# Kernel tuning notes

Hardware: AMD Instinct MI355X
Metric: run time of the kernel (lower is better)

Reference implementation:

```python
import jax, jax.numpy as jnp
import numpy as np

B, N, M = 16, 2048, 2048


def setup_inputs() -> dict:
    key = jax.random.key(0)
    k1, k2, k3 = jax.random.split(key, 3)
    pred_dsmat = jax.random.uniform(k1, (B, N, M), dtype=jnp.float32)
    # valid sizes: src_ns <= tgt_ns so a permutation GT exists for every valid row
    src_ns = jax.random.randint(k2, (B,), 1024, 1537, dtype=jnp.int32)
    tgt_ns = jax.random.randint(k3, (B,), 1537, 2049, dtype=jnp.int32)
    # gt_perm: identity permutation restricted to the valid region (one 1 per valid row)
    i = jnp.arange(N)[:, None]
    j = jnp.arange(M)[None, :]
    eye = (i == j).astype(jnp.float32)  # [N, M]
    row_mask = (jnp.arange(N)[None, :] < src_ns[:, None]).astype(jnp.float32)  # [B, N]
    gt_perm = eye[None, :, :] * row_mask[:, :, None]  # [B, N, M]
    return {"pred_dsmat": pred_dsmat, "gt_perm": gt_perm,
            "src_ns": src_ns, "tgt_ns": tgt_ns, "beta_value": 0.1}


def reference(pred_dsmat, gt_perm, src_ns, tgt_ns, beta_value):
    Bn, Nn, Mn = pred_dsmat.shape
    row_mask = jnp.arange(Nn)[None, :] < src_ns[:, None]   # [B, N] bool
    col_mask = jnp.arange(Mn)[None, :] < tgt_ns[:, None]   # [B, M] bool
    mask = row_mask[:, :, None] & col_mask[:, None, :]     # [B, N, M]

    pred = jnp.clip(pred_dsmat, 0.0, 1.0) * mask
    gt = gt_perm * mask

    gt_pred = pred * gt                      # gt-selected predicted values
    row_gt = gt_pred.sum(axis=2)             # [B, N] per-row GT value
    col_gt = gt_pred.sum(axis=1)             # [B, M] per-col GT value
    row_cnt = gt.sum(axis=2)                 # [B, N] #GT matches per row
    col_cnt = gt.sum(axis=1)                 # [B, M] #GT matches per col

    # attention masks: entries >= (gt value - beta), restricted to valid region
    att_src = ((pred >= row_gt[:, :, None] - beta_value) & mask) * row_cnt[:, :, None]
    att_tgt = ((pred >= col_gt[:, None, :] - beta_value) & mask) * col_cnt[:, None, :]

    src_neg = jnp.sum(((att_src - gt) * pred) ** 2, axis=2)  # [B, N]
    src_pos = jnp.sum(gt_pred ** 2, axis=2)                  # [B, N]
    tgt_neg = jnp.sum(((att_tgt - gt) * pred) ** 2, axis=1)  # [B, M]

    # sum of tgt_neg over the GT-matched column of each row == dot with column counts
    corr = jnp.einsum('bm,bm->b', tgt_neg, col_cnt)          # [B]

    denom = 1.0 + src_neg + corr[:, None]                    # [B, N]
    num = jnp.where(row_mask, src_pos, 1.0)
    den = jnp.where(row_mask, denom, 1.0)
    loss = -0.5 * jnp.sum(jnp.log(num / den) * row_mask)
    n_sum = src_ns.sum().astype(pred.dtype)
    return loss / n_sum
```

## Files before the change

### kernel.cpp

```cpp
#include <hip/hip_runtime.h>

#define B_ 16
#define N_ 2048
#define M_ 2048
#define RROWS 16
#define WROWS 4
#define CHUNK 1024
#define NCHUNK (M_ / CHUNK)
#define JCH (CHUNK / 256)
#define DROWS 32
#define DWROWS 8
#define KCAP 4

__device__ __forceinline__ float wave_sum(float v) {
#pragma unroll
    for (int off = 32; off >= 1; off >>= 1) v += __shfl_xor(v, off);
    return v;
}

extern "C" __global__ __launch_bounds__(256) void k_gt(
    const float* __restrict__ gt,
    const int* __restrict__ src_ns, const int* __restrict__ tgt_ns,
    int* __restrict__ nnz, int* __restrict__ ent_col,
    float* __restrict__ ent_val, int* flag)
{
    const int b = blockIdx.y;
    const int src = src_ns[b];
    const int band = blockIdx.x;
    if (band * RROWS >= src) return;
    const int tgt = tgt_ns[b];
    const int c0 = blockIdx.z * CHUNK;
    const int lim = tgt - c0;
    if (lim <= 0) return;
    const int jmaxL = lim >= CHUNK ? JCH : ((lim + 255) >> 8);
    const int wave = threadIdx.x >> 6, lane = threadIdx.x & 63;
    const int bc = b * (N_ * M_) + c0;

    const int row0 = band * RROWS + wave * WROWS;
    for (int r = 0; r < WROWS; ++r) {
        const int n = row0 + r;
        if (n >= src) break;
        const int ri = b * N_ + n;
        const float4* grow = (const float4*)(gt + bc + n * M_);
        for (int j = 0; j < jmaxL; ++j) {
            const int m4 = j * 64 + lane;
            const float4 g4 = grow[m4];
            if (g4.x != 0.f || g4.y != 0.f || g4.z != 0.f || g4.w != 0.f) {
                const int mb = c0 + m4 * 4;
#define GC(KK, MB) do { \
    const int c = mb + KK; \
    const float gv = g4.MB; \
    if (gv != 0.f && c < tgt) { \
        const int slot = atomicAdd(&nnz[ri], 1); \
        if (slot < KCAP) { ent_col[ri * KCAP + slot] = c; ent_val[ri * KCAP + slot] = gv; } \
        else *flag = 1; \
    } \
} while (0)
                GC(0, x); GC(1, y); GC(2, z); GC(3, w);
#undef GC
            }
        }
    }
}

extern "C" __global__ __launch_bounds__(256) void k_mid(
    const float* __restrict__ pred,
    const int* __restrict__ src_ns,
    const int* __restrict__ nnz, const int* __restrict__ ent_col,
    const float* __restrict__ ent_val, const int* flag,
    float* __restrict__ row_gt, float* __restrict__ row_cnt,
    float* __restrict__ col_gt, float* __restrict__ col_cnt)
{
    if (*flag) return;
    const int ri = blockIdx.x * 256 + threadIdx.x;
    const int b = ri >> 11, n = ri & (N_ - 1);
    if (n >= src_ns[b]) { row_gt[ri] = 0.f; row_cnt[ri] = 0.f; return; }
    const int nn0 = nnz[ri];
    const int nn = nn0 < KCAP ? nn0 : KCAP;
    float rg = 0.f, rc = 0.f;
    for (int s = 0; s < nn; ++s) {
        const int c = ent_col[ri * KCAP + s];
        const float gv = ent_val[ri * KCAP + s];
        float p = pred[b * (N_ * M_) + n * M_ + c];
        p = fminf(fmaxf(p, 0.f), 1.f);
        rg += gv * p; rc += gv;
        atomicAdd(&col_gt[b * M_ + c], gv * p);
        atomicAdd(&col_cnt[b * M_ + c], gv);
    }
    row_gt[ri] = rg; row_cnt[ri] = rc;
}

extern "C" __global__ __launch_bounds__(256) void k_p1d(
    const float* __restrict__ pred, const float* __restrict__ gt,
    const int* __restrict__ src_ns, const int* __restrict__ tgt_ns,
    const int* flag,
    float* __restrict__ row_gt, float* __restrict__ row_cnt,
    float* __restrict__ col_gt, float* __restrict__ col_cnt)
{
    if (*flag == 0) return;
    const int b = blockIdx.y;
    const int src = src_ns[b];
    const int band = blockIdx.x;
    if (band * DROWS >= src) return;
    const int tgt = tgt_ns[b];
    const int wave = threadIdx.x >> 6, lane = threadIdx.x & 63;
    const int base = b * (N_ * M_);

    float4 acg[8], accn[8];
#pragma unroll
    for (int j = 0; j < 8; ++j) { acg[j] = make_float4(0,0,0,0); accn[j] = make_float4(0,0,0,0); }

    const int row0 = band * DROWS + wave * DWROWS;
    for (int r = 0; r < DWROWS; ++r) {
        const int n = row0 + r;
        if (n >= src) break;
        const float4* prow = (const float4*)(pred + base + n * M_);
        const float4* grow = (const float4*)(gt + base + n * M_);
        float rg = 0.f, rc = 0.f;
#pragma unroll
        for (int j = 0; j < 8; ++j) {
            const int m4 = j * 64 + lane;
            const float4 p4 = prow[m4];
            const float4 g4 = grow[m4];
            const int mb = m4 * 4;
#define P1C(KK, MB) do { \
    const bool ok = (mb + KK) < tgt; \
    float p = fminf(fmaxf(p4.MB, 0.f), 1.f); p = ok ? p : 0.f; \
    const float g = ok ? g4.MB : 0.f; \
    const float gp = p * g; \
    rg += gp; rc += g; \
    acg[j].MB += gp; accn[j].MB += g; \
} while (0)
            P1C(0, x); P1C(1, y); P1C(2, z); P1C(3, w);
#undef P1C
        }
        rg = wave_sum(rg); rc = wave_sum(rc);
        if (lane == 0) { row_gt[b * N_ + n] = rg; row_cnt[b * N_ + n] = rc; }
    }

    __shared__ float4 s_cg[M_ / 4];
    __shared__ float4 s_cc[M_ / 4];
    for (int i = threadIdx.x; i < M_ / 4; i += 256) {
        s_cg[i] = make_float4(0,0,0,0);
        s_cc[i] = make_float4(0,0,0,0);
    }
    __syncthreads();
    for (int w = 0; w < 4; ++w) {
        if (wave == w) {
#pragma unroll
            for (int j = 0; j < 8; ++j) {
                const int i = j * 64 + lane;
                float4 v = s_cg[i];
                v.x += acg[j].x; v.y += acg[j].y; v.z += acg[j].z; v.w += acg[j].w;
                s_cg[i] = v;
                float4 u = s_cc[i];
                u.x += accn[j].x; u.y += accn[j].y; u.z += accn[j].z; u.w += accn[j].w;
                s_cc[i] = u;
            }
        }
        __syncthreads();
    }
    const float* fcg = (const float*)s_cg;
    const float* fcc = (const float*)s_cc;
    for (int i = threadIdx.x; i < M_; i += 256) {
        atomicAdd(&col_gt[b * M_ + i], fcg[i]);
        atomicAdd(&col_cnt[b * M_ + i], fcc[i]);
    }
}

extern "C" __global__ __launch_bounds__(256) void k_pred(
    const float* __restrict__ pred, const float* __restrict__ gt,
    const int* __restrict__ src_ns, const int* __restrict__ tgt_ns,
    const float* __restrict__ beta_p,
    const float* __restrict__ row_gt, const float* __restrict__ row_cnt,
    const float* __restrict__ col_gt, const float* __restrict__ col_cnt,
    const int* __restrict__ nnz, const int* __restrict__ ent_col,
    const float* __restrict__ ent_val, const int* flag,
    float* __restrict__ src_neg, float* __restrict__ src_pos,
    float* __restrict__ tgt_neg)
{
    const int b = blockIdx.y;
    const int src = src_ns[b];
    const int band = blockIdx.x;
    if (band * RROWS >= src) return;
    const int tgt = tgt_ns[b];
    const int c0 = blockIdx.z * CHUNK;
    const bool chunk0 = (c0 == 0);
    const int lim = tgt - c0;
    if (lim <= 0 && !chunk0) return;
    const int jmaxL = lim >= CHUNK ? JCH : (lim > 0 ? ((lim + 255) >> 8) : 0);
    const float beta = beta_p[0];
    const int wave = threadIdx.x >> 6, lane = threadIdx.x & 63;
    const int bfull = b * (N_ * M_);
    const int bc = bfull + c0;
    const bool dense = (*flag != 0);

    float4 cgb[JCH], cc[JCH], tn[JCH];
    const float4* cg4 = (const float4*)(col_gt + b * M_ + c0);
    const float4* cc4 = (const float4*)(col_cnt + b * M_ + c0);
#pragma unroll
    for (int j = 0; j < JCH; ++j) {
        float4 v = cg4[j * 64 + lane];
        v.x -= beta; v.y -= beta; v.z -= beta; v.w -= beta;
        cgb[j] = v;
        cc[j] = cc4[j * 64 + lane];
        tn[j] = make_float4(0,0,0,0);
    }

    const int row0 = band * RROWS + wave * WROWS;
    if (!dense) {
        for (int r = 0; r < WROWS; ++r) {
            const int n = row0 + r;
            if (n >= src) break;
            const int ri = b * N_ + n;
            const float rc = row_cnt[ri];
            const float rth = row_gt[ri] - beta;
            const float4* prow = (const float4*)(pred + bc + n * M_);
            float sneg = 0.f;
#pragma unroll
            for (int j = 0; j < JCH; ++j) {
                if (j < jmaxL) {
                    const int m4 = j * 64 + lane;
                    const float4 p4 = prow[m4];
                    const int mb = c0 + m4 * 4;
#define P2S(KK, MB) do { \
    const bool ok = (mb + KK) < tgt; \
    float p = fminf(fmaxf(p4.MB, 0.f), 1.f); p = ok ? p : 0.f; \
    const float as = (p >= rth) ? rc : 0.f; \
    const float ds = as * p; \
    sneg += ds * ds; \
    const float at = (p >= cgb[j].MB) ? cc[j].MB : 0.f; \
    const float d = at * p; \
    tn[j].MB += d * d; \
} while (0)
                    P2S(0, x); P2S(1, y); P2S(2, z); P2S(3, w);
#undef P2S
                }
            }
            sneg = wave_sum(sneg);
            if (lane == 0) {
                if (chunk0) {
                    float spos = 0.f;
                    const int nn0 = nnz[ri];
                    const int nn = nn0 < KCAP ? nn0 : KCAP;
                    for (int s = 0; s < nn; ++s) {
                        const int c = ent_col[ri * KCAP + s];
                        const float gv = ent_val[ri * KCAP + s];
                        float pv = pred[bfull + n * M_ + c];
                        pv = fminf(fmaxf(pv, 0.f), 1.f);
                        const float as = (pv >= rth) ? rc : 0.f;
                        const float d0 = as * pv;
                        const float d1 = (as - gv) * pv;
                        sneg += d1 * d1 - d0 * d0;
                        const float gp = gv * pv;
                        spos += gp * gp;
                        const float at = (pv >= col_gt[b * M_ + c] - beta) ? col_cnt[b * M_ + c] : 0.f;
                        const float t0 = at * pv;
                        const float t1 = (at - gv) * pv;
                        atomicAdd(&tgt_neg[b * M_ + c], t1 * t1 - t0 * t0);
                    }
                    atomicAdd(&src_pos[ri], spos);
                }
                atomicAdd(&src_neg[ri], sneg);
            }
        }
    } else {
        for (int r = 0; r < WROWS; ++r) {
            const int n = row0 + r;
            if (n >= src) break;
            const int ri = b * N_ + n;
            const float rc = row_cnt[ri];
            const float rth = row_gt[ri] - beta;
            const float4* prow = (const float4*)(pred + bc + n * M_);
            const float4* grow = (const float4*)(gt + bc + n * M_);
            float sneg = 0.f, spos = 0.f;
#pragma unroll
            for (int j = 0; j < JCH; ++j) {
                if (j < jmaxL) {
                    const int m4 = j * 64 + lane;
                    const float4 p4 = prow[m4];
                    const float4 g4 = grow[m4];
                    const int mb = c0 + m4 * 4;
#define P2D(KK, MB) do { \
    const bool ok = (mb + KK) < tgt; \
    float p = fminf(fmaxf(p4.MB, 0.f), 1.f); p = ok ? p : 0.f; \
    const float gv = ok ? g4.MB : 0.f; \
    const float as = (p >= rth) ? rc : 0.f; \
    const float ds = (as - gv) * p; \
    sneg += ds * ds; \
    const float gp = gv * p; spos += gp * gp; \
    const float at = (p >= cgb[j].MB) ? cc[j].MB : 0.f; \
    const float dt = (at - gv) * p; \
    tn[j].MB += dt * dt; \
} while (0)
                    P2D(0, x); P2D(1, y); P2D(2, z); P2D(3, w);
#undef P2D
                }
            }
            sneg = wave_sum(sneg); spos = wave_sum(spos);
            if (lane == 0) {
                atomicAdd(&src_neg[ri], sneg);
                atomicAdd(&src_pos[ri], spos);
            }
        }
    }

    __shared__ float4 s_tn[CHUNK / 4];
    for (int i = threadIdx.x; i < CHUNK / 4; i += 256) s_tn[i] = make_float4(0,0,0,0);
    __syncthreads();
    for (int w = 0; w < 4; ++w) {
        if (wave == w) {
#pragma unroll
            for (int j = 0; j < JCH; ++j) {
                const int i = j * 64 + lane;
                float4 v = s_tn[i];
                v.x += tn[j].x; v.y += tn[j].y; v.z += tn[j].z; v.w += tn[j].w;
                s_tn[i] = v;
            }
        }
        __syncthreads();
    }
    const float* ftn = (const float*)s_tn;
    for (int i = threadIdx.x; i < CHUNK; i += 256)
        atomicAdd(&tgt_neg[b * M_ + c0 + i], ftn[i]);
}

extern "C" __global__ __launch_bounds__(256) void k_final(
    const float* __restrict__ src_neg, const float* __restrict__ src_pos,
    const float* __restrict__ tgt_neg, const float* __restrict__ col_cnt,
    const int* __restrict__ src_ns, float* __restrict__ out)
{
    const int b = blockIdx.x;
    const int wave = threadIdx.x >> 6, lane = threadIdx.x & 63;
    __shared__ float sredc[4];
    __shared__ float sredl[4];

    float c = 0.f;
    for (int i = threadIdx.x; i < M_; i += 256)
        c += tgt_neg[b * M_ + i] * col_cnt[b * M_ + i];
    c = wave_sum(c);
    if (lane == 0) sredc[wave] = c;
    __syncthreads();
    const float corr = sredc[0] + sredc[1] + sredc[2] + sredc[3];

    const int src = src_ns[b];
    float ls = 0.f;
    for (int n = threadIdx.x; n < src; n += 256) {
        const float sp = src_pos[b * N_ + n];
        const float sn = src_neg[b * N_ + n];
        ls += logf(sp) - logf(1.f + sn + corr);
    }
    ls = wave_sum(ls);
    if (lane == 0) sredl[wave] = ls;
    __syncthreads();
    if (threadIdx.x == 0) {
        const float total = sredl[0] + sredl[1] + sredl[2] + sredl[3];
        float nsum = 0.f;
        for (int i = 0; i < B_; ++i) nsum += (float)src_ns[i];
        atomicAdd(out, -0.5f * total / nsum);
    }
}

extern "C" void kernel_launch(void* const* d_in, const int* in_sizes, int n_in,
                              void* d_out, int out_size, void* d_ws, size_t ws_size,
                              hipStream_t stream)
{
    const float* pred   = (const float*)d_in[0];
    const float* gtp    = (const float*)d_in[1];
    const int*   src_ns = (const int*)d_in[2];
    const int*   tgt_ns = (const int*)d_in[3];
    const float* beta   = (const float*)d_in[4];
    float* out = (float*)d_out;
    float* ws  = (float*)d_ws;

    float* col_gt  = ws;
    float* col_cnt = col_gt  + B_ * M_;
    float* tgt_neg = col_cnt + B_ * M_;
    float* src_neg = tgt_neg + B_ * M_;
    float* src_pos = src_neg + B_ * N_;
    int*   nnz     = (int*)(src_pos + B_ * N_);
    int*   flag    = nnz + B_ * N_;
    float* row_gt  = (float*)(flag + 1);
    float* row_cnt = row_gt + B_ * N_;
    int*   ent_col = (int*)(row_cnt + B_ * N_);
    float* ent_val = (float*)(ent_col + B_ * N_ * KCAP);

    const size_t zero_bytes = (size_t)(3 * B_ * M_ + 3 * B_ * N_ + 1) * sizeof(float);
    hipMemsetAsync(d_ws, 0, zero_bytes, stream);
    hipMemsetAsync(d_out, 0, sizeof(float), stream);

    dim3 gsplit(N_ / RROWS, B_, NCHUNK);
    k_gt<<<gsplit, 256, 0, stream>>>(gtp, src_ns, tgt_ns, nnz, ent_col, ent_val, flag);
    k_mid<<<(B_ * N_) / 256, 256, 0, stream>>>(pred, src_ns, nnz, ent_col, ent_val, flag,
                                               row_gt, row_cnt, col_gt, col_cnt);
    k_p1d<<<dim3(N_ / DROWS, B_), 256, 0, stream>>>(pred, gtp, src_ns, tgt_ns, flag,
                                                    row_gt, row_cnt, col_gt, col_cnt);
    k_pred<<<gsplit, 256, 0, stream>>>(pred, gtp, src_ns, tgt_ns, beta,
                                       row_gt, row_cnt, col_gt, col_cnt,
                                       nnz, ent_col, ent_val, flag,
                                       src_neg, src_pos, tgt_neg);
    k_final<<<B_, 256, 0, stream>>>(src_neg, src_pos, tgt_neg, col_cnt, src_ns, out);
}
```

Measured before the change: 518.0 us.

## Fold tgt_neg into per-batch corr dot product inside k_pred and unroll loads

The per-column tgt_neg array is no longer built. Each block multiplies its per-lane column partials by col_cnt, reduces them to a scalar, and issues one atomicAdd into a per-batch corr value. This removes the shared-memory serial merge and the 1024 per-block global atomics that k_pred used to do. Row loads in k_gt and k_pred are now fully unrolled into four float4 loads without the tail-chunk guard, so every row reads the whole chunk even past tgt. k_final is split into four blocks per batch.

```diff
diff --git a/kernel.cpp b/kernel.cpp
--- a/kernel.cpp
+++ b/kernel.cpp
@@ -30,9 +30,7 @@
     if (band * RROWS >= src) return;
     const int tgt = tgt_ns[b];
     const int c0 = blockIdx.z * CHUNK;
-    const int lim = tgt - c0;
-    if (lim <= 0) return;
-    const int jmaxL = lim >= CHUNK ? JCH : ((lim + 255) >> 8);
+    if (tgt - c0 <= 0) return;
     const int wave = threadIdx.x >> 6, lane = threadIdx.x & 63;
     const int bc = b * (N_ * M_) + c0;
 
@@ -42,24 +40,27 @@
         if (n >= src) break;
         const int ri = b * N_ + n;
         const float4* grow = (const float4*)(gt + bc + n * M_);
-        for (int j = 0; j < jmaxL; ++j) {
-            const int m4 = j * 64 + lane;
-            const float4 g4 = grow[m4];
-            if (g4.x != 0.f || g4.y != 0.f || g4.z != 0.f || g4.w != 0.f) {
-                const int mb = c0 + m4 * 4;
-#define GC(KK, MB) do { \
+        const float4 g0 = grow[lane];
+        const float4 g1 = grow[64 + lane];
+        const float4 g2 = grow[128 + lane];
+        const float4 g3 = grow[192 + lane];
+#define GTEST(GV, J) \
+        if (GV.x != 0.f || GV.y != 0.f || GV.z != 0.f || GV.w != 0.f) { \
+            const int mb = c0 + (J * 64 + lane) * 4; \
+            GC(GV, 0, x); GC(GV, 1, y); GC(GV, 2, z); GC(GV, 3, w); \
+        }
+#define GC(GV, KK, MB) do { \
     const int c = mb + KK; \
-    const float gv = g4.MB; \
+    const float gv = GV.MB; \
     if (gv != 0.f && c < tgt) { \
         const int slot = atomicAdd(&nnz[ri], 1); \
         if (slot < KCAP) { ent_col[ri * KCAP + slot] = c; ent_val[ri * KCAP + slot] = gv; } \
         else *flag = 1; \
     } \
 } while (0)
-                GC(0, x); GC(1, y); GC(2, z); GC(3, w);
+        GTEST(g0, 0) GTEST(g1, 1) GTEST(g2, 2) GTEST(g3, 3)
 #undef GC
-            }
-        }
+#undef GTEST
     }
 }
 
@@ -177,7 +178,7 @@
     const int* __restrict__ nnz, const int* __restrict__ ent_col,
     const float* __restrict__ ent_val, const int* flag,
     float* __restrict__ src_neg, float* __restrict__ src_pos,
-    float* __restrict__ tgt_neg)
+    float* __restrict__ corr)
 {
     const int b = blockIdx.y;
     const int src = src_ns[b];
@@ -186,9 +187,7 @@
     const int tgt = tgt_ns[b];
     const int c0 = blockIdx.z * CHUNK;
     const bool chunk0 = (c0 == 0);
-    const int lim = tgt - c0;
-    if (lim <= 0 && !chunk0) return;
-    const int jmaxL = lim >= CHUNK ? JCH : (lim > 0 ? ((lim + 255) >> 8) : 0);
+    if (tgt - c0 <= 0 && !chunk0) return;
     const float beta = beta_p[0];
     const int wave = threadIdx.x >> 6, lane = threadIdx.x & 63;
     const int bfull = b * (N_ * M_);
@@ -207,6 +206,7 @@
         tn[j] = make_float4(0,0,0,0);
     }
 
+    float cadd = 0.f;
     const int row0 = band * RROWS + wave * WROWS;
     if (!dense) {
         for (int r = 0; r < WROWS; ++r) {
@@ -216,27 +216,25 @@
             const float rc = row_cnt[ri];
             const float rth = row_gt[ri] - beta;
             const float4* prow = (const float4*)(pred + bc + n * M_);
+            const float4 p0 = prow[lane];
+            const float4 p1 = prow[64 + lane];
+            const float4 p2 = prow[128 + lane];
+            const float4 p3 = prow[192 + lane];
             float sneg = 0.f;
-#pragma unroll
-            for (int j = 0; j < JCH; ++j) {
-                if (j < jmaxL) {
-                    const int m4 = j * 64 + lane;
-                    const float4 p4 = prow[m4];
-                    const int mb = c0 + m4 * 4;
-#define P2S(KK, MB) do { \
-    const bool ok = (mb + KK) < tgt; \
-    float p = fminf(fmaxf(p4.MB, 0.f), 1.f); p = ok ? p : 0.f; \
+#define P2S(PV, J, KK, MB) do { \
+    const bool ok = (c0 + (J * 64 + lane) * 4 + KK) < tgt; \
+    float p = fminf(fmaxf(PV.MB, 0.f), 1.f); p = ok ? p : 0.f; \
     const float as = (p >= rth) ? rc : 0.f; \
     const float ds = as * p; \
     sneg += ds * ds; \
-    const float at = (p >= cgb[j].MB) ? cc[j].MB : 0.f; \
+    const float at = (p >= cgb[J].MB) ? cc[J].MB : 0.f; \
     const float d = at * p; \
-    tn[j].MB += d * d; \
+    tn[J].MB += d * d; \
 } while (0)
-                    P2S(0, x); P2S(1, y); P2S(2, z); P2S(3, w);
+#define P2SV(PV, J) P2S(PV, J, 0, x); P2S(PV, J, 1, y); P2S(PV, J, 2, z); P2S(PV, J, 3, w);
+            P2SV(p0, 0) P2SV(p1, 1) P2SV(p2, 2) P2SV(p3, 3)
+#undef P2SV
 #undef P2S
-                }
-            }
             sneg = wave_sum(sneg);
             if (lane == 0) {
                 if (chunk0) {
@@ -254,10 +252,11 @@
                         sneg += d1 * d1 - d0 * d0;
                         const float gp = gv * pv;
                         spos += gp * gp;
-                        const float at = (pv >= col_gt[b * M_ + c] - beta) ? col_cnt[b * M_ + c] : 0.f;
+                        const float ccv = col_cnt[b * M_ + c];
+                        const float at = (pv >= col_gt[b * M_ + c] - beta) ? ccv : 0.f;
                         const float t0 = at * pv;
                         const float t1 = (at - gv) * pv;
-                        atomicAdd(&tgt_neg[b * M_ + c], t1 * t1 - t0 * t0);
+                        cadd += (t1 * t1 - t0 * t0) * ccv;
                     }
                     atomicAdd(&src_pos[ri], spos);
                 }
@@ -273,30 +272,31 @@
             const float rth = row_gt[ri] - beta;
             const float4* prow = (const float4*)(pred + bc + n * M_);
             const float4* grow = (const float4*)(gt + bc + n * M_);
+            const float4 p0 = prow[lane];
+            const float4 p1 = prow[64 + lane];
+            const float4 p2 = prow[128 + lane];
+            const float4 p3 = prow[192 + lane];
+            const float4 g0 = grow[lane];
+            const float4 g1 = grow[64 + lane];
+            const float4 g2 = grow[128 + lane];
+            const float4 g3 = grow[192 + lane];
             float sneg = 0.f, spos = 0.f;
-#pragma unroll
-            for (int j = 0; j < JCH; ++j) {
-                if (j < jmaxL) {
-                    const int m4 = j * 64 + lane;
-                    const float4 p4 = prow[m4];
-                    const float4 g4 = grow[m4];
-                    const int mb = c0 + m4 * 4;
-#define P2D(KK, MB) do { \
-    const bool ok = (mb + KK) < tgt; \
-    float p = fminf(fmaxf(p4.MB, 0.f), 1.f); p = ok ? p : 0.f; \
-    const float gv = ok ? g4.MB : 0.f; \
+#define P2D(PV, GV, J, KK, MB) do { \
+    const bool ok = (c0 + (J * 64 + lane) * 4 + KK) < tgt; \
+    float p = fminf(fmaxf(PV.MB, 0.f), 1.f); p = ok ? p : 0.f; \
+    const float gv = ok ? GV.MB : 0.f; \
     const float as = (p >= rth) ? rc : 0.f; \
     const float ds = (as - gv) * p; \
     sneg += ds * ds; \
     const float gp = gv * p; spos += gp * gp; \
-    const float at = (p >= cgb[j].MB) ? cc[j].MB : 0.f; \
+    const float at = (p >= cgb[J].MB) ? cc[J].MB : 0.f; \
     const float dt = (at - gv) * p; \
-    tn[j].MB += dt * dt; \
+    tn[J].MB += dt * dt; \
 } while (0)
-                    P2D(0, x); P2D(1, y); P2D(2, z); P2D(3, w);
+#define P2DV(PV, GV, J) P2D(PV, GV, J, 0, x); P2D(PV, GV, J, 1, y); P2D(PV, GV, J, 2, z); P2D(PV, GV, J, 3, w);
+            P2DV(p0, g0, 0) P2DV(p1, g1, 1) P2DV(p2, g2, 2) P2DV(p3, g3, 3)
+#undef P2DV
 #undef P2D
-                }
-            }
             sneg = wave_sum(sneg); spos = wave_sum(spos);
             if (lane == 0) {
                 atomicAdd(&src_neg[ri], sneg);
@@ -305,52 +305,39 @@
         }
     }
 
-    __shared__ float4 s_tn[CHUNK / 4];
-    for (int i = threadIdx.x; i < CHUNK / 4; i += 256) s_tn[i] = make_float4(0,0,0,0);
+    float dp = cadd;
+#pragma unroll
+    for (int j = 0; j < JCH; ++j)
+        dp += tn[j].x * cc[j].x + tn[j].y * cc[j].y + tn[j].z * cc[j].z + tn[j].w * cc[j].w;
+    dp = wave_sum(dp);
+    __shared__ float sred[4];
+    if (lane == 0) sred[wave] = dp;
     __syncthreads();
-    for (int w = 0; w < 4; ++w) {
-        if (wave == w) {
-#pragma unroll
-            for (int j = 0; j < JCH; ++j) {
-                const int i = j * 64 + lane;
-                float4 v = s_tn[i];
-                v.x += tn[j].x; v.y += tn[j].y; v.z += tn[j].z; v.w += tn[j].w;
-                s_tn[i] = v;
-            }
-        }
-        __syncthreads();
-    }
-    const float* ftn = (const float*)s_tn;
-    for (int i = threadIdx.x; i < CHUNK; i += 256)
-        atomicAdd(&tgt_neg[b * M_ + c0 + i], ftn[i]);
+    if (threadIdx.x == 0)
+        atomicAdd(&corr[b], sred[0] + sred[1] + sred[2] + sred[3]);
 }
 
 extern "C" __global__ __launch_bounds__(256) void k_final(
     const float* __restrict__ src_neg, const float* __restrict__ src_pos,
-    const float* __restrict__ tgt_neg, const float* __restrict__ col_cnt,
-    const int* __restrict__ src_ns, float* __restrict__ out)
-{
-    const int b = blockIdx.x;
+    const float* __restrict__ corr_p, const int* __restrict__ src_ns,
+    float* __restrict__ out)
+{
+    const int b = blockIdx.x >> 2;
+    const int part = blockIdx.x & 3;
     const int wave = threadIdx.x >> 6, lane = threadIdx.x & 63;
-    __shared__ float sredc[4];
-    __shared__ float sredl[4];
-
-    float c = 0.f;
-    for (int i = threadIdx.x; i < M_; i += 256)
-        c += tgt_neg[b * M_ + i] * col_cnt[b * M_ + i];
-    c = wave_sum(c);
-    if (lane == 0) sredc[wave] = c;
-    __syncthreads();
-    const float corr = sredc[0] + sredc[1] + sredc[2] + sredc[3];
-
     const int src = src_ns[b];
+    const int n0 = part * (N_ / 4);
+    const int n1 = n0 + (N_ / 4);
+    const float corr = corr_p[b];
+
     float ls = 0.f;
-    for (int n = threadIdx.x; n < src; n += 256) {
+    for (int n = n0 + threadIdx.x; n < n1 && n < src; n += 256) {
         const float sp = src_pos[b * N_ + n];
         const float sn = src_neg[b * N_ + n];
         ls += logf(sp) - logf(1.f + sn + corr);
     }
     ls = wave_sum(ls);
+    __shared__ float sredl[4];
     if (lane == 0) sredl[wave] = ls;
     __syncthreads();
     if (threadIdx.x == 0) {
@@ -375,17 +362,17 @@
 
     float* col_gt  = ws;
     float* col_cnt = col_gt  + B_ * M_;
-    float* tgt_neg = col_cnt + B_ * M_;
-    float* src_neg = tgt_neg + B_ * M_;
+    float* src_neg = col_cnt + B_ * M_;
     float* src_pos = src_neg + B_ * N_;
-    int*   nnz     = (int*)(src_pos + B_ * N_);
+    float* corr    = src_pos + B_ * N_;
+    int*   nnz     = (int*)(corr + B_);
     int*   flag    = nnz + B_ * N_;
     float* row_gt  = (float*)(flag + 1);
     float* row_cnt = row_gt + B_ * N_;
     int*   ent_col = (int*)(row_cnt + B_ * N_);
     float* ent_val = (float*)(ent_col + B_ * N_ * KCAP);
 
-    const size_t zero_bytes = (size_t)(3 * B_ * M_ + 3 * B_ * N_ + 1) * sizeof(float);
+    const size_t zero_bytes = (size_t)(2 * B_ * M_ + 3 * B_ * N_ + B_ + 1) * sizeof(float);
     hipMemsetAsync(d_ws, 0, zero_bytes, stream);
     hipMemsetAsync(d_out, 0, sizeof(float), stream);
 
@@ -398,6 +385,6 @@
     k_pred<<<gsplit, 256, 0, stream>>>(pred, gtp, src_ns, tgt_ns, beta,
                                        row_gt, row_cnt, col_gt, col_cnt,
                                        nnz, ent_col, ent_val, flag,
-                                       src_neg, src_pos, tgt_neg);
-    k_final<<<B_, 256, 0, stream>>>(src_neg, src_pos, tgt_neg, col_cnt, src_ns, out);
-}
+                                       src_neg, src_pos, corr);
+    k_final<<<B_ * 4, 256, 0, stream>>>(src_neg, src_pos, corr, src_ns, out);
+}
```

Result: faster. 500.0 us (-3.5%).
